# Kernel tuning notes

Measured on AMD Instinct MI355X. Metric: run time of the kernel, lower is better.

The kernel has to match this reference:

```python
import jax, jax.numpy as jnp
import numpy as np

I_DIM = 20000        # item (node) count; emb_mat has I_DIM+1 rows
EMB_DIM = 128        # input embedding dim
D_DIM = 128          # hidden (scaled) dim
N_EDGES = 640000     # number of (src, dst) edges


def setup_inputs() -> dict:
    key = jax.random.key(0)
    k1, k2, k3, k4 = jax.random.split(key, 4)
    emb_mat = jax.random.normal(k1, (I_DIM + 1, EMB_DIM), dtype=jnp.float32)
    # edges must be sorted by source node (column 0) so that the original
    # tf.repeat(segment_sums, bincount(src)) trick is well-defined.
    edge = jax.random.randint(k2, (N_EDGES, 2), 0, I_DIM + 1, dtype=jnp.int64)
    order = jnp.argsort(edge[:, 0])
    edge = edge[order]
    W_scale = jax.random.normal(k3, (EMB_DIM, D_DIM), dtype=jnp.float32) * 0.05
    b_scale = jnp.zeros((D_DIM,), dtype=jnp.float32)
    W_att = jax.random.normal(k4, (2 * D_DIM, 1), dtype=jnp.float32) * 0.05
    b_att = jnp.zeros((1,), dtype=jnp.float32)
    return {"emb_mat": emb_mat, "edge": edge, "W_scale": W_scale,
            "b_scale": b_scale, "W_att": W_att, "b_att": b_att}


def reference(emb_mat, edge, W_scale, b_scale, W_att, b_att):
    num_segments = emb_mat.shape[0]          # i_dim + 1
    seg = edge[:, 0]                         # source nodes (segment ids), [E]

    # gather both endpoints, scale: [E, 2, emb] -> [E, 2, d]
    edge_emb = emb_mat[edge] @ W_scale + b_scale
    E = edge_emb.shape[0]
    # attention logit per edge from concatenated endpoint features
    att = (edge_emb.reshape(E, -1) @ W_att + b_att)[:, 0]   # [E]
    att = jax.nn.leaky_relu(att, negative_slope=0.2)
    scores = jnp.exp(att - 1.0)                              # exp(att - ones)

    # manual segment softmax over edges grouped by source node
    score_sum = jax.ops.segment_sum(scores, seg, num_segments=num_segments)
    score_norm = scores / score_sum[seg]                     # [E]

    # scale all node embeddings once, gather destination features
    item_scaled = emb_mat @ W_scale + b_scale                # [N, d]
    items = item_scaled[edge[:, 1]]                          # [E, d]

    agg = jax.ops.segment_sum(score_norm[:, None] * items, seg,
                              num_segments=num_segments)     # [N, d]
    return jax.nn.sigmoid(agg)
```

## Files before the change

kernel.cpp:

```cpp
#include <hip/hip_runtime.h>
#include <math.h>

#define NSEG 20001
#define EMB  128
#define NE   640000

#define SCALE_BLOCKS 313
#define BOUNDS_BLOCKS 2500
#define LDSL 129

__device__ __forceinline__ float dot4(float4 a, float4 b) {
    return a.x*b.x + a.y*b.y + a.z*b.z + a.w*b.w;
}

#define FMA4(acc, s, b) { acc.x += (s)*(b).x; acc.y += (s)*(b).y; acc.z += (s)*(b).z; acc.w += (s)*(b).w; }

__device__ __forceinline__ unsigned f2bf(float x) {
    unsigned u = __float_as_uint(x);
    return (u + 0x7fffu + ((u >> 16) & 1u)) >> 16;
}

__global__ __launch_bounds__(256) void prep_kernel(
    const float* __restrict__ emb, const float* __restrict__ W,
    const float* __restrict__ bsc, const float* __restrict__ Watt,
    const int* __restrict__ edge,
    unsigned short* __restrict__ tab,
    float* __restrict__ a_src, float* __restrict__ a_dst,
    int* __restrict__ seg_start, int* __restrict__ dst)
{
    const int tid = threadIdx.x;
    if (blockIdx.x >= SCALE_BLOCKS) {
        int e = (blockIdx.x - SCALE_BLOCKS) * 256 + tid;
        int2 p = ((const int2*)edge)[e];
        dst[e] = p.y;
        int sp = __shfl_up(p.x, 1);
        if ((tid & 63) == 0) sp = (e == 0) ? -1 : edge[2*e - 2];
        for (int t = sp + 1; t <= p.x; ++t) seg_start[t] = e;
        if (e == NE - 1) {
            for (int t = p.x + 1; t <= NSEG; ++t) seg_start[t] = NE;
        }
        return;
    }

    __shared__ float emb_s[64 * LDSL];
    const int r0 = blockIdx.x * 64;

    const float4* embg4 = (const float4*)emb;
    const int gmax = NSEG * 32 - 1;
    #pragma unroll
    for (int j = 0; j < 8; ++j) {
        int idx = tid + j * 256;
        int row = idx >> 5, f4 = idx & 31;
        int g = r0 * 32 + idx;
        float4 v = embg4[g <= gmax ? g : gmax];
        float* p = &emb_s[row * LDSL + f4 * 4];
        p[0] = v.x; p[1] = v.y; p[2] = v.z; p[3] = v.w;
    }
    __syncthreads();

    const int cg   = tid & 15;
    const int rowb = (tid >> 4) * 4;

    float4 accA[4] = {{0,0,0,0},{0,0,0,0},{0,0,0,0},{0,0,0,0}};
    float4 accB[4] = {{0,0,0,0},{0,0,0,0},{0,0,0,0},{0,0,0,0}};
    const float4* Wg4 = (const float4*)W;

    #pragma unroll 4
    for (int k = 0; k < EMB; ++k) {
        float4 w0 = Wg4[k*32 + cg*2];
        float4 w1 = Wg4[k*32 + cg*2 + 1];
        float a0 = emb_s[(rowb+0)*LDSL + k];
        float a1 = emb_s[(rowb+1)*LDSL + k];
        float a2 = emb_s[(rowb+2)*LDSL + k];
        float a3 = emb_s[(rowb+3)*LDSL + k];
        FMA4(accA[0], a0, w0); FMA4(accB[0], a0, w1);
        FMA4(accA[1], a1, w0); FMA4(accB[1], a1, w1);
        FMA4(accA[2], a2, w0); FMA4(accB[2], a2, w1);
        FMA4(accA[3], a3, w0); FMA4(accB[3], a3, w1);
    }

    const float4 bsA = *(const float4*)&bsc[cg*8];
    const float4 bsB = *(const float4*)&bsc[cg*8 + 4];
    const float4 wsA = *(const float4*)&Watt[cg*8];
    const float4 wsB = *(const float4*)&Watt[cg*8 + 4];
    const float4 wdA = *(const float4*)&Watt[EMB + cg*8];
    const float4 wdB = *(const float4*)&Watt[EMB + cg*8 + 4];

    #pragma unroll
    for (int r = 0; r < 4; ++r) {
        float4 A = accA[r], B = accB[r];
        A.x += bsA.x; A.y += bsA.y; A.z += bsA.z; A.w += bsA.w;
        B.x += bsB.x; B.y += bsB.y; B.z += bsB.z; B.w += bsB.w;
        const int row = r0 + rowb + r;

        if (row < NSEG) {
            uint4 pkt;
            pkt.x = f2bf(A.x) | (f2bf(A.y) << 16);
            pkt.y = f2bf(A.z) | (f2bf(A.w) << 16);
            pkt.z = f2bf(B.x) | (f2bf(B.y) << 16);
            pkt.w = f2bf(B.z) | (f2bf(B.w) << 16);
            ((uint4*)tab)[row * 16 + cg] = pkt;
        }

        float ps = dot4(A, wsA) + dot4(B, wsB);
        float pd = dot4(A, wdA) + dot4(B, wdB);
        #pragma unroll
        for (int off = 8; off >= 1; off >>= 1) {
            ps += __shfl_xor(ps, off);
            pd += __shfl_xor(pd, off);
        }
        if (cg == 0 && row < NSEG) { a_src[row] = ps; a_dst[row] = pd; }
    }
}

__device__ __forceinline__ float bf_lo(unsigned u) { return __uint_as_float(u << 16); }
__device__ __forceinline__ float bf_hi(unsigned u) { return __uint_as_float(u & 0xffff0000u); }
__device__ __forceinline__ float bcastf(float v, int j) {
    return __uint_as_float(__builtin_amdgcn_readlane(__float_as_uint(v), j));
}

__global__ __launch_bounds__(256) void agg_kernel(
    const int* __restrict__ dst, const float* __restrict__ a_src,
    const float* __restrict__ a_dst, const float* __restrict__ b_att,
    const int* __restrict__ seg_start, const unsigned int* __restrict__ tab32,
    float* __restrict__ out)
{
    const int wid = blockIdx.x * 4 + (threadIdx.x >> 6);
    if (wid >= NSEG) return;
    const int lane = threadIdx.x & 63;
    const unsigned int* tabl = tab32 + lane;

    const int s0 = seg_start[wid];
    const int s1 = seg_start[wid + 1];
    const float aS = a_src[wid] + b_att[0];

    float accx = 0.f, accy = 0.f, ssum = 0.f;

    for (int cb = s0; cb < s1; cb += 64) {
        int n = s1 - cb; if (n > 64) n = 64;
        int e = cb + lane;
        int dmine = 0; float sc = 0.f;
        if (lane < n) {
            dmine = dst[e] << 6;
            float att = aS + a_dst[dmine >> 6];
            att = att > 0.f ? att : 0.2f * att;
            sc  = expf(att - 1.f);
        }
        ssum += sc;

        int j = 0;
        for (; j + 7 < n; j += 8) {
            float w0 = bcastf(sc, j+0), w1 = bcastf(sc, j+1);
            float w2 = bcastf(sc, j+2), w3 = bcastf(sc, j+3);
            float w4 = bcastf(sc, j+4), w5 = bcastf(sc, j+5);
            float w6 = bcastf(sc, j+6), w7 = bcastf(sc, j+7);
            int d0 = __builtin_amdgcn_readlane(dmine, j+0);
            int d1 = __builtin_amdgcn_readlane(dmine, j+1);
            int d2 = __builtin_amdgcn_readlane(dmine, j+2);
            int d3 = __builtin_amdgcn_readlane(dmine, j+3);
            int d4 = __builtin_amdgcn_readlane(dmine, j+4);
            int d5 = __builtin_amdgcn_readlane(dmine, j+5);
            int d6 = __builtin_amdgcn_readlane(dmine, j+6);
            int d7 = __builtin_amdgcn_readlane(dmine, j+7);
            unsigned u0 = tabl[d0], u1 = tabl[d1], u2 = tabl[d2], u3 = tabl[d3];
            unsigned u4 = tabl[d4], u5 = tabl[d5], u6 = tabl[d6], u7 = tabl[d7];
            accx += w0 * bf_lo(u0); accy += w0 * bf_hi(u0);
            accx += w1 * bf_lo(u1); accy += w1 * bf_hi(u1);
            accx += w2 * bf_lo(u2); accy += w2 * bf_hi(u2);
            accx += w3 * bf_lo(u3); accy += w3 * bf_hi(u3);
            accx += w4 * bf_lo(u4); accy += w4 * bf_hi(u4);
            accx += w5 * bf_lo(u5); accy += w5 * bf_hi(u5);
            accx += w6 * bf_lo(u6); accy += w6 * bf_hi(u6);
            accx += w7 * bf_lo(u7); accy += w7 * bf_hi(u7);
        }
        for (; j < n; ++j) {
            float w = bcastf(sc, j);
            int   d = __builtin_amdgcn_readlane(dmine, j);
            unsigned u = tabl[d];
            accx += w * bf_lo(u);
            accy += w * bf_hi(u);
        }
    }

    #pragma unroll
    for (int off = 32; off >= 1; off >>= 1) ssum += __shfl_xor(ssum, off);

    const float inv = (s1 > s0) ? 1.f / ssum : 0.f;
    float ox = accx * inv, oy = accy * inv;
    ox = 1.f / (1.f + expf(-ox));
    oy = 1.f / (1.f + expf(-oy));
    *(float2*)&out[wid * EMB + 2 * lane] = make_float2(ox, oy);
}

extern "C" void kernel_launch(void* const* d_in, const int* in_sizes, int n_in,
                              void* d_out, int out_size, void* d_ws, size_t ws_size,
                              hipStream_t stream) {
    const float* emb  = (const float*)d_in[0];
    const int*   edge = (const int*)  d_in[1];
    const float* W    = (const float*)d_in[2];
    const float* bsc  = (const float*)d_in[3];
    const float* Watt = (const float*)d_in[4];
    const float* batt = (const float*)d_in[5];
    float* out = (float*)d_out;

    unsigned short* tab = (unsigned short*)d_ws;
    float* a_src = (float*)(tab + (size_t)NSEG * EMB);
    float* a_dst = a_src + NSEG;
    int*   seg_start = (int*)(a_dst + NSEG);
    int*   dstc = seg_start + NSEG + 3;

    prep_kernel<<<SCALE_BLOCKS + BOUNDS_BLOCKS, 256, 0, stream>>>(
        emb, W, bsc, Watt, edge, tab, a_src, a_dst, seg_start, dstc);
    agg_kernel<<<(NSEG + 3) / 4, 256, 0, stream>>>(
        dstc, a_src, a_dst, batt, seg_start, (const unsigned int*)tab, out);
}
```

Baseline: 112.8 us.

## Compute node scaling GEMM with split-bf16 MFMA and permuted feature layout

Replaces the FP32 FMA loop for emb@W_scale with bf16 MFMA 16x16x32, using a hi/lo split (three products) so the result stays close to fp32. A small new kernel pre-converts W into transposed hi/lo bf16 tiles in the workspace, and attention logits are reduced across waves through shared memory. The table now packs columns c and c+64 into each 32-bit word, so the aggregate kernel writes outputs as two strided scalars instead of float2. This adds a kernel launch and uses a fixed workspace offset, with some extra rounding error.

```diff
diff --git a/kernel.cpp b/kernel.cpp
--- a/kernel.cpp
+++ b/kernel.cpp
@@ -7,21 +7,37 @@
 
 #define SCALE_BLOCKS 313
 #define BOUNDS_BLOCKS 2500
-#define LDSL 129
-
-__device__ __forceinline__ float dot4(float4 a, float4 b) {
-    return a.x*b.x + a.y*b.y + a.z*b.z + a.w*b.w;
-}
-
-#define FMA4(acc, s, b) { acc.x += (s)*(b).x; acc.y += (s)*(b).y; acc.z += (s)*(b).z; acc.w += (s)*(b).w; }
+#define APAD 136
+
+typedef __attribute__((ext_vector_type(8))) short bf16x8;
+typedef __attribute__((ext_vector_type(4))) float f32x4;
 
 __device__ __forceinline__ unsigned f2bf(float x) {
     unsigned u = __float_as_uint(x);
     return (u + 0x7fffu + ((u >> 16) & 1u)) >> 16;
 }
+__device__ __forceinline__ float bfbits2f(unsigned h) { return __uint_as_float(h << 16); }
+
+__global__ __launch_bounds__(256) void wconv_kernel(
+    const float* __restrict__ W,
+    unsigned short* __restrict__ wt_hi, unsigned short* __restrict__ wt_lo)
+{
+    const int c  = blockIdx.x * 8 + (threadIdx.x & 7);
+    const int k0 = (threadIdx.x >> 3) * 4;
+    unsigned h[4], l[4];
+    #pragma unroll
+    for (int i = 0; i < 4; ++i) {
+        float x = W[(k0 + i) * EMB + c];
+        h[i] = f2bf(x);
+        l[i] = f2bf(x - bfbits2f(h[i]));
+    }
+    *(uint2*)&wt_hi[c * EMB + k0] = make_uint2(h[0] | (h[1] << 16), h[2] | (h[3] << 16));
+    *(uint2*)&wt_lo[c * EMB + k0] = make_uint2(l[0] | (l[1] << 16), l[2] | (l[3] << 16));
+}
 
 __global__ __launch_bounds__(256) void prep_kernel(
-    const float* __restrict__ emb, const float* __restrict__ W,
+    const float* __restrict__ emb,
+    const unsigned short* __restrict__ wt_hi, const unsigned short* __restrict__ wt_lo,
     const float* __restrict__ bsc, const float* __restrict__ Watt,
     const int* __restrict__ edge,
     unsigned short* __restrict__ tab,
@@ -42,8 +58,16 @@
         return;
     }
 
-    __shared__ float emb_s[64 * LDSL];
-    const int r0 = blockIdx.x * 64;
+    __shared__ unsigned short Ah[64 * APAD];
+    __shared__ unsigned short Al[64 * APAD];
+    __shared__ float ps_part[4][64];
+    __shared__ float pd_part[4][64];
+
+    const int r0   = blockIdx.x * 64;
+    const int w    = tid >> 6;
+    const int lane = tid & 63;
+    const int l15  = lane & 15;
+    const int lk   = lane >> 4;
 
     const float4* embg4 = (const float4*)emb;
     const int gmax = NSEG * 32 - 1;
@@ -53,63 +77,79 @@
         int row = idx >> 5, f4 = idx & 31;
         int g = r0 * 32 + idx;
         float4 v = embg4[g <= gmax ? g : gmax];
-        float* p = &emb_s[row * LDSL + f4 * 4];
-        p[0] = v.x; p[1] = v.y; p[2] = v.z; p[3] = v.w;
+        unsigned h0 = f2bf(v.x), h1 = f2bf(v.y), h2 = f2bf(v.z), h3 = f2bf(v.w);
+        unsigned l0 = f2bf(v.x - bfbits2f(h0)), l1 = f2bf(v.y - bfbits2f(h1));
+        unsigned l2 = f2bf(v.z - bfbits2f(h2)), l3 = f2bf(v.w - bfbits2f(h3));
+        int o = row * APAD + f4 * 4;
+        *(uint2*)&Ah[o] = make_uint2(h0 | (h1 << 16), h2 | (h3 << 16));
+        *(uint2*)&Al[o] = make_uint2(l0 | (l1 << 16), l2 | (l3 << 16));
     }
     __syncthreads();
 
-    const int cg   = tid & 15;
-    const int rowb = (tid >> 4) * 4;
-
-    float4 accA[4] = {{0,0,0,0},{0,0,0,0},{0,0,0,0},{0,0,0,0}};
-    float4 accB[4] = {{0,0,0,0},{0,0,0,0},{0,0,0,0},{0,0,0,0}};
-    const float4* Wg4 = (const float4*)W;
-
-    #pragma unroll 4
-    for (int k = 0; k < EMB; ++k) {
-        float4 w0 = Wg4[k*32 + cg*2];
-        float4 w1 = Wg4[k*32 + cg*2 + 1];
-        float a0 = emb_s[(rowb+0)*LDSL + k];
-        float a1 = emb_s[(rowb+1)*LDSL + k];
-        float a2 = emb_s[(rowb+2)*LDSL + k];
-        float a3 = emb_s[(rowb+3)*LDSL + k];
-        FMA4(accA[0], a0, w0); FMA4(accB[0], a0, w1);
-        FMA4(accA[1], a1, w0); FMA4(accB[1], a1, w1);
-        FMA4(accA[2], a2, w0); FMA4(accB[2], a2, w1);
-        FMA4(accA[3], a3, w0); FMA4(accB[3], a3, w1);
-    }
-
-    const float4 bsA = *(const float4*)&bsc[cg*8];
-    const float4 bsB = *(const float4*)&bsc[cg*8 + 4];
-    const float4 wsA = *(const float4*)&Watt[cg*8];
-    const float4 wsB = *(const float4*)&Watt[cg*8 + 4];
-    const float4 wdA = *(const float4*)&Watt[EMB + cg*8];
-    const float4 wdB = *(const float4*)&Watt[EMB + cg*8 + 4];
-
-    #pragma unroll
-    for (int r = 0; r < 4; ++r) {
-        float4 A = accA[r], B = accB[r];
-        A.x += bsA.x; A.y += bsA.y; A.z += bsA.z; A.w += bsA.w;
-        B.x += bsB.x; B.y += bsB.y; B.z += bsB.z; B.w += bsB.w;
-        const int row = r0 + rowb + r;
-
+    const int c0 = w * 16 + l15;
+    const int c1 = c0 + 64;
+    const bf16x8* Bh0p = (const bf16x8*)&wt_hi[c0 * EMB];
+    const bf16x8* Bh1p = (const bf16x8*)&wt_hi[c1 * EMB];
+    const bf16x8* Bl0p = (const bf16x8*)&wt_lo[c0 * EMB];
+    const bf16x8* Bl1p = (const bf16x8*)&wt_lo[c1 * EMB];
+
+    f32x4 acc[4][2];
+    #pragma unroll
+    for (int m = 0; m < 4; ++m) {
+        acc[m][0] = (f32x4){0.f, 0.f, 0.f, 0.f};
+        acc[m][1] = (f32x4){0.f, 0.f, 0.f, 0.f};
+    }
+
+    #pragma unroll
+    for (int kt = 0; kt < 4; ++kt) {
+        const int fo = kt * 4 + lk;
+        bf16x8 Bh0 = Bh0p[fo], Bh1 = Bh1p[fo];
+        bf16x8 Bl0 = Bl0p[fo], Bl1 = Bl1p[fo];
+        #pragma unroll
+        for (int m = 0; m < 4; ++m) {
+            const int ao = (m * 16 + l15) * APAD + kt * 32 + lk * 8;
+            bf16x8 Af = *(const bf16x8*)&Ah[ao];
+            bf16x8 Lf = *(const bf16x8*)&Al[ao];
+            acc[m][0] = __builtin_amdgcn_mfma_f32_16x16x32_bf16(Af, Bh0, acc[m][0], 0, 0, 0);
+            acc[m][1] = __builtin_amdgcn_mfma_f32_16x16x32_bf16(Af, Bh1, acc[m][1], 0, 0, 0);
+            acc[m][0] = __builtin_amdgcn_mfma_f32_16x16x32_bf16(Lf, Bh0, acc[m][0], 0, 0, 0);
+            acc[m][1] = __builtin_amdgcn_mfma_f32_16x16x32_bf16(Lf, Bh1, acc[m][1], 0, 0, 0);
+            acc[m][0] = __builtin_amdgcn_mfma_f32_16x16x32_bf16(Af, Bl0, acc[m][0], 0, 0, 0);
+            acc[m][1] = __builtin_amdgcn_mfma_f32_16x16x32_bf16(Af, Bl1, acc[m][1], 0, 0, 0);
+        }
+    }
+
+    const float bs0 = bsc[c0],        bs1 = bsc[c1];
+    const float ws0 = Watt[c0],       ws1 = Watt[c1];
+    const float wd0 = Watt[EMB + c0], wd1 = Watt[EMB + c1];
+
+    #pragma unroll
+    for (int m = 0; m < 4; ++m) {
+        #pragma unroll
+        for (int r = 0; r < 4; ++r) {
+            float v0 = acc[m][0][r] + bs0;
+            float v1 = acc[m][1][r] + bs1;
+            const int rl  = m * 16 + lk * 4 + r;
+            const int row = r0 + rl;
+            if (row < NSEG)
+                ((unsigned*)tab)[row * 64 + c0] = f2bf(v0) | (f2bf(v1) << 16);
+            float ps = v0 * ws0 + v1 * ws1;
+            float pd = v0 * wd0 + v1 * wd1;
+            #pragma unroll
+            for (int off = 8; off >= 1; off >>= 1) {
+                ps += __shfl_xor(ps, off);
+                pd += __shfl_xor(pd, off);
+            }
+            if (l15 == 0) { ps_part[w][rl] = ps; pd_part[w][rl] = pd; }
+        }
+    }
+    __syncthreads();
+    if (tid < 64) {
+        const int row = r0 + tid;
         if (row < NSEG) {
-            uint4 pkt;
-            pkt.x = f2bf(A.x) | (f2bf(A.y) << 16);
-            pkt.y = f2bf(A.z) | (f2bf(A.w) << 16);
-            pkt.z = f2bf(B.x) | (f2bf(B.y) << 16);
-            pkt.w = f2bf(B.z) | (f2bf(B.w) << 16);
-            ((uint4*)tab)[row * 16 + cg] = pkt;
-        }
-
-        float ps = dot4(A, wsA) + dot4(B, wsB);
-        float pd = dot4(A, wdA) + dot4(B, wdB);
-        #pragma unroll
-        for (int off = 8; off >= 1; off >>= 1) {
-            ps += __shfl_xor(ps, off);
-            pd += __shfl_xor(pd, off);
-        }
-        if (cg == 0 && row < NSEG) { a_src[row] = ps; a_dst[row] = pd; }
+            a_src[row] = ps_part[0][tid] + ps_part[1][tid] + ps_part[2][tid] + ps_part[3][tid];
+            a_dst[row] = pd_part[0][tid] + pd_part[1][tid] + pd_part[2][tid] + pd_part[3][tid];
+        }
     }
 }
 
@@ -189,7 +229,8 @@
     float ox = accx * inv, oy = accy * inv;
     ox = 1.f / (1.f + expf(-ox));
     oy = 1.f / (1.f + expf(-oy));
-    *(float2*)&out[wid * EMB + 2 * lane] = make_float2(ox, oy);
+    out[wid * EMB + lane]      = ox;
+    out[wid * EMB + 64 + lane] = oy;
 }
 
 extern "C" void kernel_launch(void* const* d_in, const int* in_sizes, int n_in,
@@ -208,9 +249,12 @@
     float* a_dst = a_src + NSEG;
     int*   seg_start = (int*)(a_dst + NSEG);
     int*   dstc = seg_start + NSEG + 3;
-
+    unsigned short* wt_hi = (unsigned short*)((char*)d_ws + (32u << 20));
+    unsigned short* wt_lo = wt_hi + EMB * EMB;
+
+    wconv_kernel<<<16, 256, 0, stream>>>(W, wt_hi, wt_lo);
     prep_kernel<<<SCALE_BLOCKS + BOUNDS_BLOCKS, 256, 0, stream>>>(
-        emb, W, bsc, Watt, edge, tab, a_src, a_dst, seg_start, dstc);
+        emb, wt_hi, wt_lo, bsc, Watt, edge, tab, a_src, a_dst, seg_start, dstc);
     agg_kernel<<<(NSEG + 3) / 4, 256, 0, stream>>>(
         dstc, a_src, a_dst, batt, seg_start, (const unsigned int*)tab, out);
 }
```

After: 107.6 us. 1.05x faster.
